# Kernel tuning notes

Measured on AMD Instinct MI355X. Metric: run time of the kernel, lower is better.

Reference implementation:

```python
import jax, jax.numpy as jnp
import numpy as np

TWO_PI = 2.0 * np.pi


def setup_inputs() -> dict:
    key = jax.random.key(0)
    k1, k2 = jax.random.split(key)
    B, N, F = 1, 4096, 4096
    query_points = jax.random.normal(k1, (B, N, 3), dtype=jnp.float32)
    face_coord = jax.random.normal(k2, (B, F, 3, 3), dtype=jnp.float32)
    return {"query_points": query_points, "face_coord": face_coord}


def _winding(query_points, face_coord):
    # query_points: [B, N, 3]; face_coord: [B, F, 3, 3]
    # Per-pair vectors from query point to each triangle vertex: [B, N, F, 3]
    qp = query_points[:, :, None, :]  # [B, N, 1, 3]
    a = face_coord[:, None, :, 0, :] - qp
    b = face_coord[:, None, :, 1, :] - qp
    c = face_coord[:, None, :, 2, :] - qp

    det = jnp.sum(a * jnp.cross(b, c), axis=-1)          # [B, N, F]
    na = jnp.linalg.norm(a, axis=-1)
    nb = jnp.linalg.norm(b, axis=-1)
    nc = jnp.linalg.norm(c, axis=-1)
    ab = jnp.sum(a * b, axis=-1)
    bc = jnp.sum(b * c, axis=-1)
    ac = jnp.sum(a * c, axis=-1)

    denom = na * nb * nc + bc * na + ac * nb + ab * nc
    solid_angle_2 = jnp.arctan2(det, denom)              # [B, N, F]
    # Sum solid angles over all faces, normalize by 2*pi -> winding number/occupancy
    return jnp.sum(solid_angle_2, axis=-1) / TWO_PI      # [B, N]


def reference(query_points, face_coord):
    return _winding(query_points, face_coord)
```

## Files before the change

kernel.cpp:

```cpp
#include <hip/hip_runtime.h>
#include <math.h>

#define N_Q 4096
#define N_F 4096
#define QPT 2
#define QBLK (256 * QPT)
#define FSPLIT 128
#define FT (N_F / FSPLIT)

__device__ __forceinline__ float fast_atan2f(float y, float x) {
    const float pi   = 3.14159265358979f;
    const float pi_2 = 1.57079632679490f;
    float ax = fabsf(x), ay = fabsf(y);
    float mx = fmaxf(ax, ay), mn = fminf(ax, ay);
    float t = mn * __builtin_amdgcn_rcpf(mx);
    t = (mx == 0.0f) ? 0.0f : t;
    float s = t * t;
    float p =              -0.0117212f;
    p = fmaf(p, s,  0.05265332f);
    p = fmaf(p, s, -0.11643287f);
    p = fmaf(p, s,  0.19354346f);
    p = fmaf(p, s, -0.33262347f);
    p = fmaf(p, s,  0.99997726f);
    float r = p * t;
    r = (ay > ax) ? (pi_2 - r) : r;
    r = (x < 0.0f) ? (pi - r) : r;
    return copysignf(r, y);
}

__device__ __forceinline__ float pair_term(
    float qx, float qy, float qz,
    float v0, float v1, float v2, float v3, float v4,
    float v5, float v6, float v7, float v8)
{
    const float ax = v0 - qx, ay = v1 - qy, az = v2 - qz;
    const float bx = v3 - qx, by = v4 - qy, bz = v5 - qz;
    const float cx = v6 - qx, cy = v7 - qy, cz = v8 - qz;

    const float ux = fmaf(by, cz, -bz * cy);
    const float uy = fmaf(bz, cx, -bx * cz);
    const float uz = fmaf(bx, cy, -by * cx);
    const float det = fmaf(ax, ux, fmaf(ay, uy, az * uz));

    const float na = __builtin_amdgcn_sqrtf(fmaf(ax, ax, fmaf(ay, ay, az * az)));
    const float nb = __builtin_amdgcn_sqrtf(fmaf(bx, bx, fmaf(by, by, bz * bz)));
    const float nc = __builtin_amdgcn_sqrtf(fmaf(cx, cx, fmaf(cy, cy, cz * cz)));

    const float ab = fmaf(ax, bx, fmaf(ay, by, az * bz));
    const float bc = fmaf(bx, cx, fmaf(by, cy, bz * cz));
    const float ac = fmaf(ax, cx, fmaf(ay, cy, az * cz));

    const float denom = fmaf(na * nb, nc, fmaf(bc, na, fmaf(ac, nb, ab * nc)));
    return fast_atan2f(det, denom);
}

__global__ __launch_bounds__(256) void winding_kernel(
    const float* __restrict__ qp,
    const float* __restrict__ fc,
    float* __restrict__ out)
{
    const int q0 = blockIdx.x * QBLK + threadIdx.x;
    const int q1 = q0 + 256;
    const int f0 = blockIdx.y * FT;

    const float q0x = qp[q0 * 3 + 0], q0y = qp[q0 * 3 + 1], q0z = qp[q0 * 3 + 2];
    const float q1x = qp[q1 * 3 + 0], q1y = qp[q1 * 3 + 1], q1z = qp[q1 * 3 + 2];

    float s0 = 0.0f, s1 = 0.0f;
    #pragma unroll 4
    for (int f = 0; f < FT; ++f) {
        const float* v = fc + (size_t)(f0 + f) * 9;
        const float v0 = v[0], v1 = v[1], v2 = v[2];
        const float v3 = v[3], v4 = v[4], v5 = v[5];
        const float v6 = v[6], v7 = v[7], v8 = v[8];

        s0 += pair_term(q0x, q0y, q0z, v0, v1, v2, v3, v4, v5, v6, v7, v8);
        s1 += pair_term(q1x, q1y, q1z, v0, v1, v2, v3, v4, v5, v6, v7, v8);
    }

    const float c = 0.15915494309189535f;
    atomicAdd(&out[q0], s0 * c);
    atomicAdd(&out[q1], s1 * c);
}

extern "C" void kernel_launch(void* const* d_in, const int* in_sizes, int n_in,
                              void* d_out, int out_size, void* d_ws, size_t ws_size,
                              hipStream_t stream) {
    const float* qp = (const float*)d_in[0];
    const float* fc = (const float*)d_in[1];
    float* out = (float*)d_out;

    hipMemsetAsync(out, 0, (size_t)out_size * sizeof(float), stream);

    dim3 grid(N_Q / QBLK, FSPLIT);
    dim3 block(256);
    winding_kernel<<<grid, block, 0, stream>>>(qp, fc, out);
}
```

Baseline: 33.15 us.

## Use four queries per thread and a workspace-based two-pass reduction

```diff
diff --git a/kernel.cpp b/kernel.cpp
--- a/kernel.cpp
+++ b/kernel.cpp
@@ -3,10 +3,11 @@
 
 #define N_Q 4096
 #define N_F 4096
-#define QPT 2
+#define QPT 4
 #define QBLK (256 * QPT)
-#define FSPLIT 128
+#define FSPLIT 256
 #define FT (N_F / FSPLIT)
+#define INV_2PI 0.15915494309189535f
 
 __device__ __forceinline__ float fast_atan2f(float y, float x) {
     const float pi   = 3.14159265358979f;
@@ -54,19 +55,21 @@
     return fast_atan2f(det, denom);
 }
 
-__global__ __launch_bounds__(256) void winding_kernel(
+__global__ __launch_bounds__(256) void winding_partial(
     const float* __restrict__ qp,
     const float* __restrict__ fc,
-    float* __restrict__ out)
+    float* __restrict__ ws)
 {
     const int q0 = blockIdx.x * QBLK + threadIdx.x;
-    const int q1 = q0 + 256;
+    const int q1 = q0 + 256, q2 = q0 + 512, q3 = q0 + 768;
     const int f0 = blockIdx.y * FT;
 
-    const float q0x = qp[q0 * 3 + 0], q0y = qp[q0 * 3 + 1], q0z = qp[q0 * 3 + 2];
-    const float q1x = qp[q1 * 3 + 0], q1y = qp[q1 * 3 + 1], q1z = qp[q1 * 3 + 2];
+    const float q0x = qp[q0*3+0], q0y = qp[q0*3+1], q0z = qp[q0*3+2];
+    const float q1x = qp[q1*3+0], q1y = qp[q1*3+1], q1z = qp[q1*3+2];
+    const float q2x = qp[q2*3+0], q2y = qp[q2*3+1], q2z = qp[q2*3+2];
+    const float q3x = qp[q3*3+0], q3y = qp[q3*3+1], q3z = qp[q3*3+2];
 
-    float s0 = 0.0f, s1 = 0.0f;
+    float s0 = 0.0f, s1 = 0.0f, s2 = 0.0f, s3 = 0.0f;
     #pragma unroll 4
     for (int f = 0; f < FT; ++f) {
         const float* v = fc + (size_t)(f0 + f) * 9;
@@ -76,11 +79,58 @@
 
         s0 += pair_term(q0x, q0y, q0z, v0, v1, v2, v3, v4, v5, v6, v7, v8);
         s1 += pair_term(q1x, q1y, q1z, v0, v1, v2, v3, v4, v5, v6, v7, v8);
+        s2 += pair_term(q2x, q2y, q2z, v0, v1, v2, v3, v4, v5, v6, v7, v8);
+        s3 += pair_term(q3x, q3y, q3z, v0, v1, v2, v3, v4, v5, v6, v7, v8);
     }
 
-    const float c = 0.15915494309189535f;
-    atomicAdd(&out[q0], s0 * c);
-    atomicAdd(&out[q1], s1 * c);
+    float* w = ws + (size_t)blockIdx.y * N_Q;
+    w[q0] = s0; w[q1] = s1; w[q2] = s2; w[q3] = s3;
+}
+
+__global__ __launch_bounds__(256) void winding_reduce(
+    const float* __restrict__ ws, float* __restrict__ out)
+{
+    const int q = blockIdx.x * 256 + threadIdx.x;
+    float a0 = 0.0f, a1 = 0.0f, a2 = 0.0f, a3 = 0.0f;
+    #pragma unroll 4
+    for (int s = 0; s < FSPLIT; s += 4) {
+        a0 += ws[(size_t)(s+0) * N_Q + q];
+        a1 += ws[(size_t)(s+1) * N_Q + q];
+        a2 += ws[(size_t)(s+2) * N_Q + q];
+        a3 += ws[(size_t)(s+3) * N_Q + q];
+    }
+    out[q] = ((a0 + a1) + (a2 + a3)) * INV_2PI;
+}
+
+__global__ __launch_bounds__(256) void winding_atomic(
+    const float* __restrict__ qp, const float* __restrict__ fc,
+    float* __restrict__ out)
+{
+    const int q0 = blockIdx.x * QBLK + threadIdx.x;
+    const int q1 = q0 + 256, q2 = q0 + 512, q3 = q0 + 768;
+    const int f0 = blockIdx.y * FT;
+
+    const float q0x = qp[q0*3+0], q0y = qp[q0*3+1], q0z = qp[q0*3+2];
+    const float q1x = qp[q1*3+0], q1y = qp[q1*3+1], q1z = qp[q1*3+2];
+    const float q2x = qp[q2*3+0], q2y = qp[q2*3+1], q2z = qp[q2*3+2];
+    const float q3x = qp[q3*3+0], q3y = qp[q3*3+1], q3z = qp[q3*3+2];
+
+    float s0 = 0.0f, s1 = 0.0f, s2 = 0.0f, s3 = 0.0f;
+    #pragma unroll 4
+    for (int f = 0; f < FT; ++f) {
+        const float* v = fc + (size_t)(f0 + f) * 9;
+        const float v0 = v[0], v1 = v[1], v2 = v[2];
+        const float v3 = v[3], v4 = v[4], v5 = v[5];
+        const float v6 = v[6], v7 = v[7], v8 = v[8];
+        s0 += pair_term(q0x, q0y, q0z, v0, v1, v2, v3, v4, v5, v6, v7, v8);
+        s1 += pair_term(q1x, q1y, q1z, v0, v1, v2, v3, v4, v5, v6, v7, v8);
+        s2 += pair_term(q2x, q2y, q2z, v0, v1, v2, v3, v4, v5, v6, v7, v8);
+        s3 += pair_term(q3x, q3y, q3z, v0, v1, v2, v3, v4, v5, v6, v7, v8);
+    }
+    atomicAdd(&out[q0], s0 * INV_2PI);
+    atomicAdd(&out[q1], s1 * INV_2PI);
+    atomicAdd(&out[q2], s2 * INV_2PI);
+    atomicAdd(&out[q3], s3 * INV_2PI);
 }
 
 extern "C" void kernel_launch(void* const* d_in, const int* in_sizes, int n_in,
@@ -90,9 +140,16 @@
     const float* fc = (const float*)d_in[1];
     float* out = (float*)d_out;
 
-    hipMemsetAsync(out, 0, (size_t)out_size * sizeof(float), stream);
-
+    const size_t ws_needed = (size_t)FSPLIT * N_Q * sizeof(float);
     dim3 grid(N_Q / QBLK, FSPLIT);
     dim3 block(256);
-    winding_kernel<<<grid, block, 0, stream>>>(qp, fc, out);
+
+    if (ws_size >= ws_needed) {
+        float* ws = (float*)d_ws;
+        winding_partial<<<grid, block, 0, stream>>>(qp, fc, ws);
+        winding_reduce<<<dim3(N_Q / 256), block, 0, stream>>>(ws, out);
+    } else {
+        hipMemsetAsync(out, 0, (size_t)out_size * sizeof(float), stream);
+        winding_atomic<<<grid, block, 0, stream>>>(qp, fc, out);
+    }
 }
```

Result: slower. 46.88 us (+41.4%).
